# Kernel optimization log

Hardware: AMD Instinct MI355X
Metric: run time of the kernel (lower is better)

The kernel has to match this reference:

```python
import jax, jax.numpy as jnp
import numpy as np

FP8_MAX = 448.0
EPS = 1e-12


def setup_inputs() -> dict:
    key = jax.random.key(0)
    k1, k2 = jax.random.split(key)
    x = jax.random.normal(k1, (4, 2048, 4096), dtype=jnp.float32)
    # kaiming-uniform-like init scale for weight
    weight = jax.random.normal(k2, (4096, 4096), dtype=jnp.float32) * 0.02
    bias = jnp.zeros((4096,), dtype=jnp.float32)
    return {"x": x, "weight": weight, "bias": bias}


def reference(x, weight, bias):
    # per-tensor fake-quant of activations
    input_scale = jnp.maximum(jnp.max(jnp.abs(x)) / FP8_MAX, EPS)
    x_q = jnp.round(jnp.clip(x / input_scale, -FP8_MAX, FP8_MAX))
    # per-tensor fake-quant of weight
    weight_scale = jnp.maximum(jnp.max(jnp.abs(weight)) / FP8_MAX, EPS)
    weight_q = jnp.round(jnp.clip(weight / weight_scale, -FP8_MAX, FP8_MAX))
    # GEMM in quantized domain, then dequant rescale + bias
    out_q = jnp.einsum('bsi,oi->bso', x_q, weight_q)  # [B,S,out]
    out = (out_q * (input_scale * weight_scale)).astype(x.dtype) + bias
    return out
```

## Files before the change

kernel.cpp:

```cpp
#include <hip/hip_runtime.h>

#define FP8_MAX 448.0f
#define EPSF 1e-12f

#define BM 256
#define BN 256
#define BK 64

typedef __attribute__((ext_vector_type(8))) _Float16 half8;
typedef __attribute__((ext_vector_type(4))) float floatx4;

#define VMCNT(n) asm volatile("s_waitcnt vmcnt(" #n ")" ::: "memory")

__device__ inline void async_copy16(const void* gp, void* lp) {
  __builtin_amdgcn_global_load_lds(
      (const __attribute__((address_space(1))) unsigned int*)gp,
      (__attribute__((address_space(3))) unsigned int*)lp,
      16, 0, 0);
}

__global__ void absmax2_kernel(const float* __restrict__ a, int n4a,
                               const float* __restrict__ b, int n4b,
                               int blocks_a, unsigned* __restrict__ out) {
  const bool isA = (int)blockIdx.x < blocks_a;
  const float4* in4 = (const float4*)(isA ? a : b);
  const int n4 = isA ? n4a : n4b;
  const int nblk = isA ? blocks_a : (gridDim.x - blocks_a);
  const int bid = isA ? blockIdx.x : (blockIdx.x - blocks_a);
  int tid = bid * blockDim.x + threadIdx.x;
  int stride = nblk * blockDim.x;
  float m = 0.f;
  for (int i = tid; i < n4; i += stride) {
    float4 v = in4[i];
    m = fmaxf(m, fmaxf(fmaxf(fabsf(v.x), fabsf(v.y)),
                       fmaxf(fabsf(v.z), fabsf(v.w))));
  }
  for (int off = 32; off > 0; off >>= 1)
    m = fmaxf(m, __shfl_down(m, off, 64));
  __shared__ float smax[4];
  int lane = threadIdx.x & 63, w = threadIdx.x >> 6;
  if (lane == 0) smax[w] = m;
  __syncthreads();
  if (threadIdx.x == 0) {
    float bm = fmaxf(fmaxf(smax[0], smax[1]), fmaxf(smax[2], smax[3]));
    atomicMax(out + (isA ? 0 : 1), __float_as_uint(bm));
  }
}

__global__ void quant2_kernel(const float* __restrict__ a, int n8a,
                              const float* __restrict__ b, int n8b,
                              int blocks_a, _Float16* __restrict__ qa,
                              _Float16* __restrict__ qb,
                              const unsigned* __restrict__ amax_bits) {
  const bool isA = (int)blockIdx.x < blocks_a;
  const float4* in4 = (const float4*)(isA ? a : b);
  half8* out8 = (half8*)(isA ? qa : qb);
  const int n8 = isA ? n8a : n8b;
  const int nblk = isA ? blocks_a : (gridDim.x - blocks_a);
  const int bid = isA ? blockIdx.x : (blockIdx.x - blocks_a);
  const float scale =
      fmaxf(__uint_as_float(amax_bits[isA ? 0 : 1]) / FP8_MAX, EPSF);
  int tid = bid * blockDim.x + threadIdx.x;
  int stride = nblk * blockDim.x;
  for (int i = tid; i < n8; i += stride) {
    float4 va = in4[2 * i], vb = in4[2 * i + 1];
    half8 h;
    h[0] = (_Float16)rintf(fminf(fmaxf(va.x / scale, -FP8_MAX), FP8_MAX));
    h[1] = (_Float16)rintf(fminf(fmaxf(va.y / scale, -FP8_MAX), FP8_MAX));
    h[2] = (_Float16)rintf(fminf(fmaxf(va.z / scale, -FP8_MAX), FP8_MAX));
    h[3] = (_Float16)rintf(fminf(fmaxf(va.w / scale, -FP8_MAX), FP8_MAX));
    h[4] = (_Float16)rintf(fminf(fmaxf(vb.x / scale, -FP8_MAX), FP8_MAX));
    h[5] = (_Float16)rintf(fminf(fmaxf(vb.y / scale, -FP8_MAX), FP8_MAX));
    h[6] = (_Float16)rintf(fminf(fmaxf(vb.z / scale, -FP8_MAX), FP8_MAX));
    h[7] = (_Float16)rintf(fminf(fmaxf(vb.w / scale, -FP8_MAX), FP8_MAX));
    out8[i] = h;
  }
}

__global__ __launch_bounds__(512, 2) void gemm8_kernel(
    const _Float16* __restrict__ A,
    const _Float16* __restrict__ B,
    const float* __restrict__ bias, const unsigned* __restrict__ amax,
    float* __restrict__ C,
    int M, int N, int K) {
  __shared__ __align__(16) _Float16 As[2][BM * BK];
  __shared__ __align__(16) _Float16 Bs[2][BN * BK];

  const int tid = threadIdx.x;
  const int w = tid >> 6;
  const int lane = tid & 63;
  const int wr = w >> 2;
  const int wc = w & 3;

  const int nwg = gridDim.x;
  const int cpx = nwg >> 3;
  const int swz = (blockIdx.x & 7) * cpx + (blockIdx.x >> 3);
  const int nbn = N / BN;
  const int bm = swz / nbn;
  const int bn = swz % nbn;

  const _Float16* Ab = A + (size_t)bm * BM * K;
  const _Float16* Bb = B + (size_t)bn * BN * K;

  const int srow8 = w * 8 + (lane >> 3);
  const int gd8 = ((lane & 7) ^ ((lane >> 3) & 7)) * 8;
  const _Float16* Ag = Ab + (size_t)srow8 * K + gd8;
  const _Float16* Bg = Bb + (size_t)srow8 * K + gd8;

  auto stageA = [&](int kt, int h) {
#pragma unroll
    for (int r = 2 * h; r < 2 * h + 2; ++r)
      async_copy16(Ag + (size_t)(r * 64) * K + kt * BK,
                   (void*)&As[kt & 1][(r * 64 + w * 8) * BK]);
  };
  auto stageB = [&](int kt, int h) {
#pragma unroll
    for (int r = 2 * h; r < 2 * h + 2; ++r)
      async_copy16(Bg + (size_t)(r * 64) * K + kt * BK,
                   (void*)&Bs[kt & 1][(r * 64 + w * 8) * BK]);
  };

  const int lr = lane & 15;
  const int hi = lane >> 4;
  const int aoff = (wr * 128 + lr) * BK;
  const int boff = (wc * 64 + lr) * BK;
  const int g0 = (hi ^ (lr & 7)) * 8;
  const int g1 = ((4 + hi) ^ (lr & 7)) * 8;

  half8 aL[4][2], aH[4][2], bL[2][2], bH[2][2];
  floatx4 acc[8][4] = {};
  const int nt = K / BK;

  stageA(0, 0); stageA(0, 1); stageB(0, 0); stageB(0, 1);
  stageA(1, 0); stageA(1, 1);
  VMCNT(4);
  __builtin_amdgcn_s_barrier();

  for (int t = 0; t < nt; ++t) {
    const int b = t & 1;
    const _Float16* Asb = &As[b][0];
    const _Float16* Bsb = &Bs[b][0];

#pragma unroll
    for (int m = 0; m < 4; ++m) {
      aL[m][0] = *(const half8*)&Asb[aoff + m * 16 * BK + g0];
      aL[m][1] = *(const half8*)&Asb[aoff + m * 16 * BK + g1];
    }
#pragma unroll
    for (int n = 0; n < 2; ++n) {
      bL[n][0] = *(const half8*)&Bsb[boff + n * 16 * BK + g0];
      bL[n][1] = *(const half8*)&Bsb[boff + n * 16 * BK + g1];
    }
    if (t + 1 < nt) stageB(t + 1, 0);
    __builtin_amdgcn_s_barrier();
    __builtin_amdgcn_s_setprio(1);
#pragma unroll
    for (int m = 0; m < 4; ++m)
#pragma unroll
      for (int n = 0; n < 2; ++n)
#pragma unroll
        for (int kk = 0; kk < 2; ++kk)
          acc[m][n] = __builtin_amdgcn_mfma_f32_16x16x32_f16(
              aL[m][kk], bL[n][kk], acc[m][n], 0, 0, 0);
    __builtin_amdgcn_s_setprio(0);
    __builtin_amdgcn_s_barrier();

#pragma unroll
    for (int m = 0; m < 4; ++m) {
      aH[m][0] = *(const half8*)&Asb[aoff + (64 + m * 16) * BK + g0];
      aH[m][1] = *(const half8*)&Asb[aoff + (64 + m * 16) * BK + g1];
    }
#pragma unroll
    for (int n = 0; n < 2; ++n) {
      bH[n][0] = *(const half8*)&Bsb[boff + (32 + n * 16) * BK + g0];
      bH[n][1] = *(const half8*)&Bsb[boff + (32 + n * 16) * BK + g1];
    }
    if (t + 1 < nt) stageB(t + 1, 1);
    __builtin_amdgcn_s_barrier();
    __builtin_amdgcn_s_setprio(1);
#pragma unroll
    for (int m = 0; m < 4; ++m)
#pragma unroll
      for (int n = 0; n < 2; ++n)
#pragma unroll
        for (int kk = 0; kk < 2; ++kk)
          acc[m][2 + n] = __builtin_amdgcn_mfma_f32_16x16x32_f16(
              aL[m][kk], bH[n][kk], acc[m][2 + n], 0, 0, 0);
    __builtin_amdgcn_s_setprio(0);
    __builtin_amdgcn_s_barrier();

    if (t + 2 < nt) stageA(t + 2, 0);
    __builtin_amdgcn_s_setprio(1);
#pragma unroll
    for (int m = 0; m < 4; ++m)
#pragma unroll
      for (int n = 0; n < 2; ++n)
#pragma unroll
        for (int kk = 0; kk < 2; ++kk)
          acc[4 + m][n] = __builtin_amdgcn_mfma_f32_16x16x32_f16(
              aH[m][kk], bL[n][kk], acc[4 + m][n], 0, 0, 0);
    __builtin_amdgcn_s_setprio(0);
    __builtin_amdgcn_s_barrier();

    if (t + 2 < nt) stageA(t + 2, 1);
    __builtin_amdgcn_s_setprio(1);
#pragma unroll
    for (int m = 0; m < 4; ++m)
#pragma unroll
      for (int n = 0; n < 2; ++n)
#pragma unroll
        for (int kk = 0; kk < 2; ++kk)
          acc[4 + m][2 + n] = __builtin_amdgcn_mfma_f32_16x16x32_f16(
              aH[m][kk], bH[n][kk], acc[4 + m][2 + n], 0, 0, 0);
    __builtin_amdgcn_s_setprio(0);
    if (t + 2 < nt) {
      VMCNT(4);
    } else {
      VMCNT(0);
    }
    __builtin_amdgcn_s_barrier();
  }

  const float sx = fmaxf(__uint_as_float(amax[0]) / FP8_MAX, EPSF);
  const float sw = fmaxf(__uint_as_float(amax[1]) / FP8_MAX, EPSF);
  const float s = sx * sw;

  const int row0 = bm * BM + wr * 128 + hi * 4;
  const int col0 = bn * BN + wc * 64 + lr;
  float bv[4];
#pragma unroll
  for (int n = 0; n < 4; ++n) bv[n] = bias[col0 + n * 16];

#pragma unroll
  for (int m = 0; m < 8; ++m) {
#pragma unroll
    for (int n = 0; n < 4; ++n) {
      const size_t base = (size_t)(row0 + m * 16) * N + col0 + n * 16;
#pragma unroll
      for (int r = 0; r < 4; ++r)
        C[base + (size_t)r * N] = acc[m][n][r] * s + bv[n];
    }
  }
}

extern "C" void kernel_launch(void* const* d_in, const int* in_sizes, int n_in,
                              void* d_out, int out_size, void* d_ws,
                              size_t ws_size, hipStream_t stream) {
  const float* x = (const float*)d_in[0];
  const float* wgt = (const float*)d_in[1];
  const float* bias = (const float*)d_in[2];
  float* out = (float*)d_out;

  const int N = in_sizes[2];
  const int K = in_sizes[1] / N;
  const int M = in_sizes[0] / K;

  unsigned* amax = (unsigned*)d_ws;
  _Float16* xq = (_Float16*)((char*)d_ws + 256);
  _Float16* wq =
      (_Float16*)((char*)d_ws + 256 + (size_t)M * K * sizeof(_Float16));

  hipMemsetAsync(d_ws, 0, 8, stream);
  absmax2_kernel<<<3072, 256, 0, stream>>>(x, M * K / 4, wgt, N * K / 4, 2048,
                                           amax);
  quant2_kernel<<<3072, 256, 0, stream>>>(x, M * K / 8, wgt, N * K / 8, 2048,
                                          xq, wq, amax);

  gemm8_kernel<<<dim3((M / BM) * (N / BN)), 512, 0, stream>>>(
      xq, wq, bias, amax, out, M, N, K);
}
```

Baseline: 378.2 us.

## Restructure GEMM main loop to prefetch next-tile fragments and cut barriers

Each wave's output sub-tile now comes from two 128-row/128-col halves of the block tile instead of one contiguous region, and the epilogue indexing is changed to match. The main loop is reordered so the next tile's low A/B register fragments are loaded from the alternate LDS buffer during the last MFMA group. Global-to-LDS staging for B and the second A half moves to the top of each iteration, and one barrier per iteration is removed. The aim is to hide LDS read latency behind MFMAs and cut synchronisation. The trade-off is a full vmcnt(0) wait each iteration and more live registers.

```diff
diff --git a/kernel.cpp b/kernel.cpp
--- a/kernel.cpp
+++ b/kernel.cpp
@@ -122,37 +122,50 @@
 
   const int lr = lane & 15;
   const int hi = lane >> 4;
-  const int aoff = (wr * 128 + lr) * BK;
-  const int boff = (wc * 64 + lr) * BK;
   const int g0 = (hi ^ (lr & 7)) * 8;
   const int g1 = ((4 + hi) ^ (lr & 7)) * 8;
+  const int aoffL = (wr * 64 + lr) * BK;
+  const int aoffH = (128 + wr * 64 + lr) * BK;
+  const int boffL = (wc * 32 + lr) * BK;
+  const int boffH = (128 + wc * 32 + lr) * BK;
 
   half8 aL[4][2], aH[4][2], bL[2][2], bH[2][2];
   floatx4 acc[8][4] = {};
   const int nt = K / BK;
 
   stageA(0, 0); stageA(0, 1); stageB(0, 0); stageB(0, 1);
-  stageA(1, 0); stageA(1, 1);
-  VMCNT(4);
+  stageA(1, 0);
+  VMCNT(2);
   __builtin_amdgcn_s_barrier();
+#pragma unroll
+  for (int m = 0; m < 4; ++m) {
+    aL[m][0] = *(const half8*)&As[0][aoffL + m * 16 * BK + g0];
+    aL[m][1] = *(const half8*)&As[0][aoffL + m * 16 * BK + g1];
+  }
+#pragma unroll
+  for (int n = 0; n < 2; ++n) {
+    bL[n][0] = *(const half8*)&Bs[0][boffL + n * 16 * BK + g0];
+    bL[n][1] = *(const half8*)&Bs[0][boffL + n * 16 * BK + g1];
+  }
 
   for (int t = 0; t < nt; ++t) {
     const int b = t & 1;
     const _Float16* Asb = &As[b][0];
     const _Float16* Bsb = &Bs[b][0];
-
-#pragma unroll
-    for (int m = 0; m < 4; ++m) {
-      aL[m][0] = *(const half8*)&Asb[aoff + m * 16 * BK + g0];
-      aL[m][1] = *(const half8*)&Asb[aoff + m * 16 * BK + g1];
-    }
+    const _Float16* Asn = &As[b ^ 1][0];
+    const _Float16* Bsn = &Bs[b ^ 1][0];
+
 #pragma unroll
     for (int n = 0; n < 2; ++n) {
-      bL[n][0] = *(const half8*)&Bsb[boff + n * 16 * BK + g0];
-      bL[n][1] = *(const half8*)&Bsb[boff + n * 16 * BK + g1];
-    }
-    if (t + 1 < nt) stageB(t + 1, 0);
-    __builtin_amdgcn_s_barrier();
+      bH[n][0] = *(const half8*)&Bsb[boffH + n * 16 * BK + g0];
+      bH[n][1] = *(const half8*)&Bsb[boffH + n * 16 * BK + g1];
+    }
+#pragma unroll
+    for (int m = 0; m < 2; ++m) {
+      aH[m][0] = *(const half8*)&Asb[aoffH + m * 16 * BK + g0];
+      aH[m][1] = *(const half8*)&Asb[aoffH + m * 16 * BK + g1];
+    }
+    if (t + 1 < nt) { stageA(t + 1, 1); stageB(t + 1, 0); stageB(t + 1, 1); }
     __builtin_amdgcn_s_setprio(1);
 #pragma unroll
     for (int m = 0; m < 4; ++m)
@@ -166,17 +179,10 @@
     __builtin_amdgcn_s_barrier();
 
 #pragma unroll
-    for (int m = 0; m < 4; ++m) {
-      aH[m][0] = *(const half8*)&Asb[aoff + (64 + m * 16) * BK + g0];
-      aH[m][1] = *(const half8*)&Asb[aoff + (64 + m * 16) * BK + g1];
-    }
-#pragma unroll
-    for (int n = 0; n < 2; ++n) {
-      bH[n][0] = *(const half8*)&Bsb[boff + (32 + n * 16) * BK + g0];
-      bH[n][1] = *(const half8*)&Bsb[boff + (32 + n * 16) * BK + g1];
-    }
-    if (t + 1 < nt) stageB(t + 1, 1);
-    __builtin_amdgcn_s_barrier();
+    for (int m = 2; m < 4; ++m) {
+      aH[m][0] = *(const half8*)&Asb[aoffH + m * 16 * BK + g0];
+      aH[m][1] = *(const half8*)&Asb[aoffH + m * 16 * BK + g1];
+    }
     __builtin_amdgcn_s_setprio(1);
 #pragma unroll
     for (int m = 0; m < 4; ++m)
@@ -189,7 +195,6 @@
     __builtin_amdgcn_s_setprio(0);
     __builtin_amdgcn_s_barrier();
 
-    if (t + 2 < nt) stageA(t + 2, 0);
     __builtin_amdgcn_s_setprio(1);
 #pragma unroll
     for (int m = 0; m < 4; ++m)
@@ -200,9 +205,22 @@
           acc[4 + m][n] = __builtin_amdgcn_mfma_f32_16x16x32_f16(
               aH[m][kk], bL[n][kk], acc[4 + m][n], 0, 0, 0);
     __builtin_amdgcn_s_setprio(0);
-    __builtin_amdgcn_s_barrier();
-
-    if (t + 2 < nt) stageA(t + 2, 1);
+    VMCNT(0);
+    __builtin_amdgcn_s_barrier();
+
+    if (t + 1 < nt) {
+#pragma unroll
+      for (int m = 0; m < 4; ++m) {
+        aL[m][0] = *(const half8*)&Asn[aoffL + m * 16 * BK + g0];
+        aL[m][1] = *(const half8*)&Asn[aoffL + m * 16 * BK + g1];
+      }
+#pragma unroll
+      for (int n = 0; n < 2; ++n) {
+        bL[n][0] = *(const half8*)&Bsn[boffL + n * 16 * BK + g0];
+        bL[n][1] = *(const half8*)&Bsn[boffL + n * 16 * BK + g1];
+      }
+    }
+    if (t + 2 < nt) stageA(t + 2, 0);
     __builtin_amdgcn_s_setprio(1);
 #pragma unroll
     for (int m = 0; m < 4; ++m)
@@ -213,11 +231,6 @@
           acc[4 + m][2 + n] = __builtin_amdgcn_mfma_f32_16x16x32_f16(
               aH[m][kk], bH[n][kk], acc[4 + m][2 + n], 0, 0, 0);
     __builtin_amdgcn_s_setprio(0);
-    if (t + 2 < nt) {
-      VMCNT(4);
-    } else {
-      VMCNT(0);
-    }
     __builtin_amdgcn_s_barrier();
   }
 
@@ -225,17 +238,18 @@
   const float sw = fmaxf(__uint_as_float(amax[1]) / FP8_MAX, EPSF);
   const float s = sx * sw;
 
-  const int row0 = bm * BM + wr * 128 + hi * 4;
-  const int col0 = bn * BN + wc * 64 + lr;
   float bv[4];
 #pragma unroll
-  for (int n = 0; n < 4; ++n) bv[n] = bias[col0 + n * 16];
+  for (int n = 0; n < 4; ++n)
+    bv[n] = bias[bn * BN + (n >> 1) * 128 + wc * 32 + (n & 1) * 16 + lr];
 
 #pragma unroll
   for (int m = 0; m < 8; ++m) {
 #pragma unroll
     for (int n = 0; n < 4; ++n) {
-      const size_t base = (size_t)(row0 + m * 16) * N + col0 + n * 16;
+      const int row = bm * BM + (m >> 2) * 128 + wr * 64 + (m & 3) * 16 + hi * 4;
+      const int col = bn * BN + (n >> 1) * 128 + wc * 32 + (n & 1) * 16 + lr;
+      const size_t base = (size_t)row * N + col;
 #pragma unroll
       for (int r = 0; r < 4; ++r)
         C[base + (size_t)r * N] = acc[m][n][r] * s + bv[n];
```

After: 402.0 us. 6.3% more time.
